# Kernel tuning notes

Measured on AMD Instinct MI355X. Metric: run time of the kernel, lower is better.

The kernel has to match this reference:

```python
import jax, jax.numpy as jnp
import numpy as np

B, S, D, H = 64, 197, 768, 12
HD = D // H  # 64
WIN = 14
NUM_REL = (2 * WIN - 1) ** 2 + 3  # 732


def _build_rel_index():
    ch = np.arange(WIN)
    coords = np.stack(np.meshgrid(ch, ch, indexing='ij'))  # [2, W, W]
    flat = coords.reshape(2, -1)  # [2, W*W]
    rel = flat[:, :, None] - flat[:, None, :]  # [2, W*W, W*W]
    rel = rel.transpose(1, 2, 0).astype(np.int64)
    rel[:, :, 0] += WIN - 1
    rel[:, :, 1] += WIN - 1
    rel[:, :, 0] *= 2 * WIN - 1
    idx = np.zeros((WIN * WIN + 1, WIN * WIN + 1), dtype=np.int64)
    idx[1:, 1:] = rel.sum(-1)
    idx[0, :] = NUM_REL - 3
    idx[:, 0] = NUM_REL - 2
    idx[0, 0] = NUM_REL - 1
    return idx


def setup_inputs() -> dict:
    key = jax.random.key(0)
    ks = jax.random.split(key, 7)
    s = 0.02
    return {
        'hidden_states': jax.random.normal(ks[0], (B, S, D), jnp.float32),
        'wq': jax.random.normal(ks[1], (D, D), jnp.float32) * s,
        'bq': jax.random.normal(ks[2], (D,), jnp.float32) * s,
        'wk': jax.random.normal(ks[3], (D, D), jnp.float32) * s,  # key has no bias in BEiT
        'wv': jax.random.normal(ks[4], (D, D), jnp.float32) * s,
        'bv': jax.random.normal(ks[5], (D,), jnp.float32) * s,
        'bias_table': jax.random.normal(ks[6], (NUM_REL, H), jnp.float32) * s,
        'rel_index': jnp.asarray(_build_rel_index(), jnp.int32),
    }


def reference(hidden_states, wq, bq, wk, wv, bv, bias_table, rel_index):
    def heads(x):  # [B,S,D] -> [B,H,S,HD]
        return x.reshape(B, S, H, HD).transpose(0, 2, 1, 3)

    q = heads(hidden_states @ wq.T + bq)
    k = heads(hidden_states @ wk.T)
    v = heads(hidden_states @ wv.T + bv)

    scale = 1.0 / jnp.sqrt(jnp.asarray(HD, hidden_states.dtype))
    scores = jnp.einsum('bhqd,bhkd->bhqk', q, k) * scale  # [B,H,S,S]

    # relative position bias: [S,S,H] -> [1,H,S,S]
    rel_bias = bias_table[rel_index].transpose(2, 0, 1)[None]
    scores = scores + rel_bias

    probs = jax.nn.softmax(scores, axis=-1)
    ctx = jnp.einsum('bhqk,bhkd->bhqd', probs, v)  # [B,H,S,HD]
    return ctx.transpose(0, 2, 1, 3).reshape(B, S, D)
```

## Files before the change

### kernel.cpp

```cpp
#include <hip/hip_runtime.h>


#define S_LEN 197
#define HEADS 12
#define HDIM 64
#define DMODEL 768
#define BATCH 64
#define MROWS (BATCH * S_LEN)
#define MPAD 12672
#define NCOLS (3 * DMODEL)
#define KDIM DMODEL
#define QKV_ELEMS ((size_t)BATCH * HEADS * S_LEN * HDIM)

#define NQT 13
#define SPAD 208
#define KS_STRIDE 72
#define VT_STRIDE 232
#define PS_STRIDE 232

typedef __attribute__((ext_vector_type(8))) short short8;
typedef __attribute__((ext_vector_type(4))) float floatx4;

__device__ __forceinline__ float bf2f(ushort u) {
  union { unsigned int i; float f; } x;
  x.i = ((unsigned int)u) << 16;
  return x.f;
}
__device__ __forceinline__ ushort f2bf(float f) {
  union { float f; unsigned int i; } x;
  x.f = f;
  unsigned int r = x.i + 0x7fffu + ((x.i >> 16) & 1u);
  return (ushort)(r >> 16);
}

__global__ void k_convert_h(const float* __restrict__ hs, ushort* __restrict__ hbf) {
  int col = blockIdx.x * 256 + threadIdx.x;
  int row = blockIdx.y;
  float v = (row < MROWS) ? hs[(size_t)row * DMODEL + col] : 0.f;
  hbf[(size_t)row * DMODEL + col] = f2bf(v);
}

__global__ void k_convert_w(const float* __restrict__ wq, const float* __restrict__ wk,
                            const float* __restrict__ wv, ushort* __restrict__ wbf) {
  int col = blockIdx.x * 256 + threadIdx.x;
  int row = blockIdx.y;
  const float* src = (row < DMODEL) ? &wq[(size_t)row * DMODEL]
                     : (row < 2 * DMODEL) ? &wk[(size_t)(row - DMODEL) * DMODEL]
                                          : &wv[(size_t)(row - 2 * DMODEL) * DMODEL];
  wbf[(size_t)row * DMODEL + col] = f2bf(src[col]);
}

__global__ void k_bias_expand(const float* __restrict__ bt, const int* __restrict__ ridx,
                              float* __restrict__ biasb) {
  int idx = blockIdx.x * 256 + threadIdx.x;
  if (idx >= HEADS * S_LEN * S_LEN) return;
  int h = idx / (S_LEN * S_LEN);
  int r = idx - h * (S_LEN * S_LEN);
  biasb[idx] = bt[ridx[r] * HEADS + h];
}

__global__ __launch_bounds__(256) void k_gemm_qkv(
    const ushort* __restrict__ A, const ushort* __restrict__ W,
    const float* __restrict__ bq, const float* __restrict__ bv,
    ushort* __restrict__ Qb, ushort* __restrict__ Kb, ushort* __restrict__ Vb) {
  __shared__ __align__(16) ushort As[128 * 40];
  __shared__ __align__(16) ushort Bs[128 * 40];
  int tid = threadIdx.x;
  int wave = tid >> 6, lane = tid & 63;
  int quad = lane >> 4, l16 = lane & 15;
  int m0 = blockIdx.y * 128, n0 = blockIdx.x * 128;
  int wm = (wave & 1) * 64, wn = (wave >> 1) * 64;

  floatx4 acc[4][4];
  floatx4 z = {0.f, 0.f, 0.f, 0.f};
#pragma unroll
  for (int i = 0; i < 4; ++i)
#pragma unroll
    for (int j = 0; j < 4; ++j) acc[i][j] = z;

  for (int kb = 0; kb < KDIM; kb += 32) {
#pragma unroll
    for (int s = 0; s < 2; ++s) {
      int c = tid + s * 256;
      int row = c >> 2;
      int kc = (c & 3) * 8;
      *(uint4*)(&As[row * 40 + kc]) =
          *(const uint4*)(&A[(size_t)(m0 + row) * KDIM + kb + kc]);
      *(uint4*)(&Bs[row * 40 + kc]) =
          *(const uint4*)(&W[(size_t)(n0 + row) * KDIM + kb + kc]);
    }
    __syncthreads();
    short8 af[4], bfr[4];
#pragma unroll
    for (int i = 0; i < 4; ++i) {
      af[i] = *(const short8*)(&As[(wm + i * 16 + l16) * 40 + quad * 8]);
      bfr[i] = *(const short8*)(&Bs[(wn + i * 16 + l16) * 40 + quad * 8]);
    }
#pragma unroll
    for (int i = 0; i < 4; ++i)
#pragma unroll
      for (int j = 0; j < 4; ++j)
        acc[i][j] = __builtin_amdgcn_mfma_f32_16x16x32_bf16(af[i], bfr[j], acc[i][j], 0, 0, 0);
    __syncthreads();
  }

#pragma unroll
  for (int j = 0; j < 4; ++j) {
    int col = n0 + wn + j * 16 + l16;
    int which = col / DMODEL;
    int rem = col - which * DMODEL;
    int hh = rem >> 6;
    int d = rem & 63;
    float bias = (which == 0) ? bq[col] : ((which == 2) ? bv[col - 2 * DMODEL] : 0.f);
    ushort* dst = (which == 0) ? Qb : ((which == 1) ? Kb : Vb);
#pragma unroll
    for (int i = 0; i < 4; ++i) {
#pragma unroll
      for (int r = 0; r < 4; ++r) {
        int m = m0 + wm + i * 16 + quad * 4 + r;
        if (m < MROWS) {
          int bb = m / S_LEN;
          int ss = m - bb * S_LEN;
          dst[((size_t)(bb * HEADS + hh) * S_LEN + ss) * HDIM + d] =
              f2bf(acc[i][j][r] + bias);
        }
      }
    }
  }
}

__global__ __launch_bounds__(512) void k_attn_mfma(
    const ushort* __restrict__ Qb, const ushort* __restrict__ Kb,
    const ushort* __restrict__ Vb, const float* __restrict__ biasb,
    float* __restrict__ out) {
  __shared__ __align__(16) ushort Ks[SPAD * KS_STRIDE];
  __shared__ __align__(16) ushort Vt[HDIM * VT_STRIDE];
  __shared__ __align__(16) ushort Ps[8 * 16 * PS_STRIDE];
  int bh = blockIdx.x;
  int b = bh / HEADS, h = bh - b * HEADS;
  int tid = threadIdx.x;
  int wave = tid >> 6, lane = tid & 63;
  int quad = lane >> 4, l16 = lane & 15;

  {
    uint4 z4 = {0u, 0u, 0u, 0u};
    for (int i = tid; i < SPAD * KS_STRIDE / 8; i += 512) ((uint4*)Ks)[i] = z4;
    for (int i = tid; i < HDIM * VT_STRIDE / 8; i += 512) ((uint4*)Vt)[i] = z4;
    for (int i = tid; i < 8 * 16 * PS_STRIDE / 8; i += 512) ((uint4*)Ps)[i] = z4;
  }
  __syncthreads();

  const ushort* Kg = Kb + (size_t)bh * S_LEN * HDIM;
  const ushort* Vg = Vb + (size_t)bh * S_LEN * HDIM;
  for (int idx = tid; idx < S_LEN * HDIM; idx += 512) {
    int key = idx >> 6, d = idx & 63;
    Ks[key * KS_STRIDE + d] = Kg[idx];
    Vt[d * VT_STRIDE + key] = Vg[idx];
  }
  __syncthreads();

  const ushort* Qg = Qb + (size_t)bh * S_LEN * HDIM;
  const float* biasH = biasb + (size_t)h * S_LEN * S_LEN;
  ushort* Psw = Ps + wave * 16 * PS_STRIDE;

  for (int qt = wave; qt < NQT; qt += 8) {
    int q0 = qt * 16;
    short8 qa0 = *(const short8*)&Qg[(q0 + l16) * HDIM + quad * 8];
    short8 qa1 = *(const short8*)&Qg[(q0 + l16) * HDIM + 32 + quad * 8];

    floatx4 brow[NQT];
    int qrow = q0 + quad * 4;
#pragma unroll
    for (int kt = 0; kt < NQT; ++kt) {
      int key = kt * 16 + l16;
      int keyc = (key < S_LEN) ? key : (S_LEN - 1);
#pragma unroll
      for (int r = 0; r < 4; ++r) {
        int q = qrow + r;
        int qc = (q < S_LEN) ? q : (S_LEN - 1);
        float bv = biasH[qc * S_LEN + keyc];
        brow[kt][r] = (q < S_LEN && key < S_LEN) ? bv : -1e30f;
      }
    }

    floatx4 sacc[NQT];
    floatx4 zz = {0.f, 0.f, 0.f, 0.f};
#pragma unroll
    for (int kt = 0; kt < NQT; ++kt) sacc[kt] = zz;
#pragma unroll
    for (int kt = 0; kt < NQT; ++kt) {
      short8 kb0 = *(const short8*)&Ks[(kt * 16 + l16) * KS_STRIDE + quad * 8];
      short8 kb1 = *(const short8*)&Ks[(kt * 16 + l16) * KS_STRIDE + 32 + quad * 8];
      sacc[kt] = __builtin_amdgcn_mfma_f32_16x16x32_bf16(qa0, kb0, sacc[kt], 0, 0, 0);
      sacc[kt] = __builtin_amdgcn_mfma_f32_16x16x32_bf16(qa1, kb1, sacc[kt], 0, 0, 0);
    }

    float mx[4] = {-3e38f, -3e38f, -3e38f, -3e38f};
#pragma unroll
    for (int kt = 0; kt < NQT; ++kt)
#pragma unroll
      for (int r = 0; r < 4; ++r) {
        float s = sacc[kt][r] * 0.125f + brow[kt][r];
        sacc[kt][r] = s;
        mx[r] = fmaxf(mx[r], s);
      }
#pragma unroll
    for (int r = 0; r < 4; ++r) {
      mx[r] = fmaxf(mx[r], __shfl_xor(mx[r], 1));
      mx[r] = fmaxf(mx[r], __shfl_xor(mx[r], 2));
      mx[r] = fmaxf(mx[r], __shfl_xor(mx[r], 4));
      mx[r] = fmaxf(mx[r], __shfl_xor(mx[r], 8));
    }
    float sum[4] = {0.f, 0.f, 0.f, 0.f};
#pragma unroll
    for (int kt = 0; kt < NQT; ++kt)
#pragma unroll
      for (int r = 0; r < 4; ++r) {
        float e = __expf(sacc[kt][r] - mx[r]);
        sum[r] += e;
        Psw[(quad * 4 + r) * PS_STRIDE + kt * 16 + l16] = f2bf(e);
      }
#pragma unroll
    for (int r = 0; r < 4; ++r) {
      sum[r] += __shfl_xor(sum[r], 1);
      sum[r] += __shfl_xor(sum[r], 2);
      sum[r] += __shfl_xor(sum[r], 4);
      sum[r] += __shfl_xor(sum[r], 8);
    }
    float inv[4];
#pragma unroll
    for (int r = 0; r < 4; ++r) inv[r] = 1.f / sum[r];

    floatx4 oacc[4];
#pragma unroll
    for (int dt = 0; dt < 4; ++dt) oacc[dt] = zz;
#pragma unroll
    for (int kk = 0; kk < 7; ++kk) {
      short8 pa = *(const short8*)&Psw[l16 * PS_STRIDE + kk * 32 + quad * 8];
#pragma unroll
      for (int dt = 0; dt < 4; ++dt) {
        short8 vb = *(const short8*)&Vt[(dt * 16 + l16) * VT_STRIDE + kk * 32 + quad * 8];
        oacc[dt] = __builtin_amdgcn_mfma_f32_16x16x32_bf16(pa, vb, oacc[dt], 0, 0, 0);
      }
    }

    float* outg = out + (size_t)b * S_LEN * DMODEL + h * HDIM;
#pragma unroll
    for (int dt = 0; dt < 4; ++dt) {
#pragma unroll
      for (int r = 0; r < 4; ++r) {
        int q = q0 + quad * 4 + r;
        if (q < S_LEN)
          outg[(size_t)q * DMODEL + dt * 16 + l16] = oacc[dt][r] * inv[r];
      }
    }
  }
}

extern "C" void kernel_launch(void* const* d_in, const int* in_sizes, int n_in,
                              void* d_out, int out_size, void* d_ws, size_t ws_size,
                              hipStream_t stream) {
  const float* hs = (const float*)d_in[0];
  const float* wq = (const float*)d_in[1];
  const float* bq = (const float*)d_in[2];
  const float* wk = (const float*)d_in[3];
  const float* wv = (const float*)d_in[4];
  const float* bv = (const float*)d_in[5];
  const float* bt = (const float*)d_in[6];
  const int* ridx = (const int*)d_in[7];
  float* out = (float*)d_out;

  ushort* hbf = (ushort*)d_ws;
  ushort* wbf = hbf + (size_t)MPAD * KDIM;
  ushort* Qb = wbf + (size_t)NCOLS * KDIM;
  ushort* Kb = Qb + QKV_ELEMS;
  ushort* Vb = Kb + QKV_ELEMS;
  float* biasb = (float*)(Vb + QKV_ELEMS);

  k_convert_h<<<dim3(3, MPAD), 256, 0, stream>>>(hs, hbf);
  k_convert_w<<<dim3(3, NCOLS), 256, 0, stream>>>(wq, wk, wv, wbf);
  int nb = (HEADS * S_LEN * S_LEN + 255) / 256;
  k_bias_expand<<<nb, 256, 0, stream>>>(bt, ridx, biasb);
  k_gemm_qkv<<<dim3(NCOLS / 128, MPAD / 128), 256, 0, stream>>>(hbf, wbf, bq, bv, Qb, Kb, Vb);
  k_attn_mfma<<<BATCH * HEADS, 512, 0, stream>>>(Qb, Kb, Vb, biasb, out);
}
```

Measured before the change: 251.4 us.

## Split attention key tiles across waves and use async LDS loads in QKV GEMM

The QKV GEMM now stages its tiles with global_load_lds direct-to-LDS loads into an XOR-swizzled 32-wide layout instead of padded register round-trips, and folds the 1/sqrt(d) scale into the Q projection. The attention kernel now has four waves cooperate on each 16-query tile, splitting the key tiles among them. K is read straight from global memory, the bias is fed in as the MFMA accumulator init, and the cross-wave max and sum reductions go through LDS with block barriers. V is transposed into a swizzled layout. The aim is more parallelism per query tile, fewer registers and less LDS traffic, at the cost of extra __syncthreads per iteration and uncached global K reads.

```diff
diff --git a/kernel.cpp b/kernel.cpp
--- a/kernel.cpp
+++ b/kernel.cpp
@@ -13,19 +13,17 @@
 #define QKV_ELEMS ((size_t)BATCH * HEADS * S_LEN * HDIM)
 
 #define NQT 13
-#define SPAD 208
-#define KS_STRIDE 72
-#define VT_STRIDE 232
-#define PS_STRIDE 232
+#define VT_ST 256
+#define P_ST 256
 
 typedef __attribute__((ext_vector_type(8))) short short8;
 typedef __attribute__((ext_vector_type(4))) float floatx4;
 
-__device__ __forceinline__ float bf2f(ushort u) {
-  union { unsigned int i; float f; } x;
-  x.i = ((unsigned int)u) << 16;
-  return x.f;
-}
+#define GLD16(gp, lp)                                                                  \
+  __builtin_amdgcn_global_load_lds(                                                    \
+      (const __attribute__((address_space(1))) unsigned int*)(gp),                     \
+      (__attribute__((address_space(3))) unsigned int*)(lp), 16, 0, 0)
+
 __device__ __forceinline__ ushort f2bf(float f) {
   union { float f; unsigned int i; } x;
   x.f = f;
@@ -63,13 +61,14 @@
     const ushort* __restrict__ A, const ushort* __restrict__ W,
     const float* __restrict__ bq, const float* __restrict__ bv,
     ushort* __restrict__ Qb, ushort* __restrict__ Kb, ushort* __restrict__ Vb) {
-  __shared__ __align__(16) ushort As[128 * 40];
-  __shared__ __align__(16) ushort Bs[128 * 40];
+  __shared__ __align__(16) ushort As[128 * 32];
+  __shared__ __align__(16) ushort Bs[128 * 32];
   int tid = threadIdx.x;
   int wave = tid >> 6, lane = tid & 63;
   int quad = lane >> 4, l16 = lane & 15;
   int m0 = blockIdx.y * 128, n0 = blockIdx.x * 128;
   int wm = (wave & 1) * 64, wn = (wave >> 1) * 64;
+  int swz = (quad ^ (l16 & 3)) << 3;
 
   floatx4 acc[4][4];
   floatx4 z = {0.f, 0.f, 0.f, 0.f};
@@ -78,23 +77,24 @@
 #pragma unroll
     for (int j = 0; j < 4; ++j) acc[i][j] = z;
 
+  int p0 = wave * 128 + lane;
   for (int kb = 0; kb < KDIM; kb += 32) {
+    const ushort* Arow = A + (size_t)m0 * KDIM + kb;
+    const ushort* Brow = W + (size_t)n0 * KDIM + kb;
 #pragma unroll
     for (int s = 0; s < 2; ++s) {
-      int c = tid + s * 256;
-      int row = c >> 2;
-      int kc = (c & 3) * 8;
-      *(uint4*)(&As[row * 40 + kc]) =
-          *(const uint4*)(&A[(size_t)(m0 + row) * KDIM + kb + kc]);
-      *(uint4*)(&Bs[row * 40 + kc]) =
-          *(const uint4*)(&W[(size_t)(n0 + row) * KDIM + kb + kc]);
+      int p = p0 + s * 64;
+      int r = p >> 2;
+      int kc = ((p ^ r) & 3) << 3;
+      GLD16(&Arow[(size_t)r * KDIM + kc], &As[p * 8]);
+      GLD16(&Brow[(size_t)r * KDIM + kc], &Bs[p * 8]);
     }
     __syncthreads();
     short8 af[4], bfr[4];
 #pragma unroll
     for (int i = 0; i < 4; ++i) {
-      af[i] = *(const short8*)(&As[(wm + i * 16 + l16) * 40 + quad * 8]);
-      bfr[i] = *(const short8*)(&Bs[(wn + i * 16 + l16) * 40 + quad * 8]);
+      af[i] = *(const short8*)(&As[(wm + i * 16 + l16) * 32 + swz]);
+      bfr[i] = *(const short8*)(&Bs[(wn + i * 16 + l16) * 32 + swz]);
     }
 #pragma unroll
     for (int i = 0; i < 4; ++i)
@@ -112,6 +112,7 @@
     int hh = rem >> 6;
     int d = rem & 63;
     float bias = (which == 0) ? bq[col] : ((which == 2) ? bv[col - 2 * DMODEL] : 0.f);
+    float scl = (which == 0) ? 0.125f : 1.0f;
     ushort* dst = (which == 0) ? Qb : ((which == 1) ? Kb : Vb);
 #pragma unroll
     for (int i = 0; i < 4; ++i) {
@@ -122,7 +123,7 @@
           int bb = m / S_LEN;
           int ss = m - bb * S_LEN;
           dst[((size_t)(bb * HEADS + hh) * S_LEN + ss) * HDIM + d] =
-              f2bf(acc[i][j][r] + bias);
+              f2bf((acc[i][j][r] + bias) * scl);
         }
       }
     }
@@ -133,125 +134,145 @@
     const ushort* __restrict__ Qb, const ushort* __restrict__ Kb,
     const ushort* __restrict__ Vb, const float* __restrict__ biasb,
     float* __restrict__ out) {
-  __shared__ __align__(16) ushort Ks[SPAD * KS_STRIDE];
-  __shared__ __align__(16) ushort Vt[HDIM * VT_STRIDE];
-  __shared__ __align__(16) ushort Ps[8 * 16 * PS_STRIDE];
+  __shared__ __align__(16) ushort Vt[HDIM * VT_ST];
+  __shared__ __align__(16) ushort Ps[2 * 16 * P_ST];
+  __shared__ __align__(16) float red[2 * 16 * 8];
   int bh = blockIdx.x;
   int b = bh / HEADS, h = bh - b * HEADS;
   int tid = threadIdx.x;
   int wave = tid >> 6, lane = tid & 63;
   int quad = lane >> 4, l16 = lane & 15;
+  int g = wave >> 2, wq = wave & 3;
 
   {
     uint4 z4 = {0u, 0u, 0u, 0u};
-    for (int i = tid; i < SPAD * KS_STRIDE / 8; i += 512) ((uint4*)Ks)[i] = z4;
-    for (int i = tid; i < HDIM * VT_STRIDE / 8; i += 512) ((uint4*)Vt)[i] = z4;
-    for (int i = tid; i < 8 * 16 * PS_STRIDE / 8; i += 512) ((uint4*)Ps)[i] = z4;
+    for (int i = tid; i < HDIM * VT_ST / 8; i += 512) ((uint4*)Vt)[i] = z4;
+    for (int i = tid; i < 2 * 16 * P_ST / 8; i += 512) ((uint4*)Ps)[i] = z4;
   }
   __syncthreads();
 
+  const ushort* Vg = Vb + (size_t)bh * S_LEN * HDIM;
+  for (int idx = tid; idx < S_LEN * 32; idx += 512) {
+    int key = idx >> 5;
+    int d = (idx & 31) * 2;
+    unsigned int v = *(const unsigned int*)&Vg[key * HDIM + d];
+    int co = key & 7, ch = key >> 3;
+    Vt[d * VT_ST + ((ch ^ (d & 7)) << 3) + co] = (ushort)(v & 0xffffu);
+    Vt[(d + 1) * VT_ST + ((ch ^ ((d + 1) & 7)) << 3) + co] = (ushort)(v >> 16);
+  }
+  __syncthreads();
+
+  const ushort* Qg = Qb + (size_t)bh * S_LEN * HDIM;
   const ushort* Kg = Kb + (size_t)bh * S_LEN * HDIM;
-  const ushort* Vg = Vb + (size_t)bh * S_LEN * HDIM;
-  for (int idx = tid; idx < S_LEN * HDIM; idx += 512) {
-    int key = idx >> 6, d = idx & 63;
-    Ks[key * KS_STRIDE + d] = Kg[idx];
-    Vt[d * VT_STRIDE + key] = Vg[idx];
-  }
-  __syncthreads();
-
-  const ushort* Qg = Qb + (size_t)bh * S_LEN * HDIM;
   const float* biasH = biasb + (size_t)h * S_LEN * S_LEN;
-  ushort* Psw = Ps + wave * 16 * PS_STRIDE;
-
-  for (int qt = wave; qt < NQT; qt += 8) {
-    int q0 = qt * 16;
-    short8 qa0 = *(const short8*)&Qg[(q0 + l16) * HDIM + quad * 8];
-    short8 qa1 = *(const short8*)&Qg[(q0 + l16) * HDIM + 32 + quad * 8];
-
-    floatx4 brow[NQT];
-    int qrow = q0 + quad * 4;
-#pragma unroll
-    for (int kt = 0; kt < NQT; ++kt) {
-      int key = kt * 16 + l16;
-      int keyc = (key < S_LEN) ? key : (S_LEN - 1);
-#pragma unroll
-      for (int r = 0; r < 4; ++r) {
-        int q = qrow + r;
-        int qc = (q < S_LEN) ? q : (S_LEN - 1);
-        float bv = biasH[qc * S_LEN + keyc];
-        brow[kt][r] = (q < S_LEN && key < S_LEN) ? bv : -1e30f;
-      }
-    }
-
-    floatx4 sacc[NQT];
-    floatx4 zz = {0.f, 0.f, 0.f, 0.f};
-#pragma unroll
-    for (int kt = 0; kt < NQT; ++kt) sacc[kt] = zz;
-#pragma unroll
-    for (int kt = 0; kt < NQT; ++kt) {
-      short8 kb0 = *(const short8*)&Ks[(kt * 16 + l16) * KS_STRIDE + quad * 8];
-      short8 kb1 = *(const short8*)&Ks[(kt * 16 + l16) * KS_STRIDE + 32 + quad * 8];
-      sacc[kt] = __builtin_amdgcn_mfma_f32_16x16x32_bf16(qa0, kb0, sacc[kt], 0, 0, 0);
-      sacc[kt] = __builtin_amdgcn_mfma_f32_16x16x32_bf16(qa1, kb1, sacc[kt], 0, 0, 0);
-    }
-
-    float mx[4] = {-3e38f, -3e38f, -3e38f, -3e38f};
-#pragma unroll
-    for (int kt = 0; kt < NQT; ++kt)
-#pragma unroll
-      for (int r = 0; r < 4; ++r) {
-        float s = sacc[kt][r] * 0.125f + brow[kt][r];
-        sacc[kt][r] = s;
-        mx[r] = fmaxf(mx[r], s);
-      }
-#pragma unroll
-    for (int r = 0; r < 4; ++r) {
-      mx[r] = fmaxf(mx[r], __shfl_xor(mx[r], 1));
-      mx[r] = fmaxf(mx[r], __shfl_xor(mx[r], 2));
-      mx[r] = fmaxf(mx[r], __shfl_xor(mx[r], 4));
-      mx[r] = fmaxf(mx[r], __shfl_xor(mx[r], 8));
-    }
-    float sum[4] = {0.f, 0.f, 0.f, 0.f};
-#pragma unroll
-    for (int kt = 0; kt < NQT; ++kt)
-#pragma unroll
-      for (int r = 0; r < 4; ++r) {
-        float e = __expf(sacc[kt][r] - mx[r]);
-        sum[r] += e;
-        Psw[(quad * 4 + r) * PS_STRIDE + kt * 16 + l16] = f2bf(e);
-      }
-#pragma unroll
-    for (int r = 0; r < 4; ++r) {
-      sum[r] += __shfl_xor(sum[r], 1);
-      sum[r] += __shfl_xor(sum[r], 2);
-      sum[r] += __shfl_xor(sum[r], 4);
-      sum[r] += __shfl_xor(sum[r], 8);
-    }
-    float inv[4];
-#pragma unroll
-    for (int r = 0; r < 4; ++r) inv[r] = 1.f / sum[r];
-
-    floatx4 oacc[4];
-#pragma unroll
-    for (int dt = 0; dt < 4; ++dt) oacc[dt] = zz;
-#pragma unroll
-    for (int kk = 0; kk < 7; ++kk) {
-      short8 pa = *(const short8*)&Psw[l16 * PS_STRIDE + kk * 32 + quad * 8];
-#pragma unroll
-      for (int dt = 0; dt < 4; ++dt) {
-        short8 vb = *(const short8*)&Vt[(dt * 16 + l16) * VT_STRIDE + kk * 32 + quad * 8];
-        oacc[dt] = __builtin_amdgcn_mfma_f32_16x16x32_bf16(pa, vb, oacc[dt], 0, 0, 0);
-      }
-    }
-
-    float* outg = out + (size_t)b * S_LEN * DMODEL + h * HDIM;
-#pragma unroll
-    for (int dt = 0; dt < 4; ++dt) {
-#pragma unroll
-      for (int r = 0; r < 4; ++r) {
-        int q = q0 + quad * 4 + r;
-        if (q < S_LEN)
-          outg[(size_t)q * DMODEL + dt * 16 + l16] = oacc[dt][r] * inv[r];
+  ushort* Pg = Ps + g * 16 * P_ST;
+  float* redg = red + g * 16 * 8;
+  int kt0 = (wq == 0) ? 0 : (3 * wq + 1);
+  int ktn = (wq == 0) ? 4 : 3;
+
+  for (int it = 0; it < 7; ++it) {
+    int qt = 2 * it + g;
+    bool active = (qt < NQT);
+    floatx4 sacc[4];
+    float mx[4];
+    if (active) {
+      int q0 = qt * 16;
+      short8 qa0 = *(const short8*)&Qg[(q0 + l16) * HDIM + quad * 8];
+      short8 qa1 = *(const short8*)&Qg[(q0 + l16) * HDIM + 32 + quad * 8];
+      int qrow = q0 + quad * 4;
+#pragma unroll
+      for (int t = 0; t < 4; ++t) {
+        if (t < ktn) {
+          int key = (kt0 + t) * 16 + l16;
+          int keyc = (key < S_LEN) ? key : (S_LEN - 1);
+          floatx4 cin;
+#pragma unroll
+          for (int r = 0; r < 4; ++r) {
+            int q = qrow + r;
+            int qc = (q < S_LEN) ? q : (S_LEN - 1);
+            float bv = biasH[qc * S_LEN + keyc];
+            cin[r] = (q < S_LEN && key < S_LEN) ? bv : -1e30f;
+          }
+          short8 kb0 = *(const short8*)&Kg[key * HDIM + quad * 8];
+          short8 kb1 = *(const short8*)&Kg[key * HDIM + 32 + quad * 8];
+          floatx4 s1 = __builtin_amdgcn_mfma_f32_16x16x32_bf16(qa0, kb0, cin, 0, 0, 0);
+          sacc[t] = __builtin_amdgcn_mfma_f32_16x16x32_bf16(qa1, kb1, s1, 0, 0, 0);
+        }
+      }
+#pragma unroll
+      for (int r = 0; r < 4; ++r) {
+        float m = -3e38f;
+#pragma unroll
+        for (int t = 0; t < 4; ++t)
+          if (t < ktn) m = fmaxf(m, sacc[t][r]);
+        m = fmaxf(m, __shfl_xor(m, 1));
+        m = fmaxf(m, __shfl_xor(m, 2));
+        m = fmaxf(m, __shfl_xor(m, 4));
+        m = fmaxf(m, __shfl_xor(m, 8));
+        mx[r] = m;
+      }
+      if (l16 == 0) {
+#pragma unroll
+        for (int r = 0; r < 4; ++r) redg[(quad * 4 + r) * 8 + wq] = mx[r];
+      }
+    }
+    __syncthreads();
+    if (active) {
+      float sum[4];
+#pragma unroll
+      for (int r = 0; r < 4; ++r) {
+        floatx4 mp = *(const floatx4*)&redg[(quad * 4 + r) * 8];
+        mx[r] = fmaxf(fmaxf(mp[0], mp[1]), fmaxf(mp[2], mp[3]));
+        sum[r] = 0.f;
+      }
+#pragma unroll
+      for (int t = 0; t < 4; ++t) {
+        if (t < ktn) {
+          int col = (kt0 + t) * 16 + l16;
+          int cpos = col >> 3, coff = col & 7;
+#pragma unroll
+          for (int r = 0; r < 4; ++r) {
+            int row = quad * 4 + r;
+            float e = __expf(sacc[t][r] - mx[r]);
+            sum[r] += e;
+            Pg[row * P_ST + ((cpos ^ (row & 7)) << 3) + coff] = f2bf(e);
+          }
+        }
+      }
+#pragma unroll
+      for (int r = 0; r < 4; ++r) {
+        float s = sum[r];
+        s += __shfl_xor(s, 1);
+        s += __shfl_xor(s, 2);
+        s += __shfl_xor(s, 4);
+        s += __shfl_xor(s, 8);
+        sum[r] = s;
+      }
+      if (l16 == 0) {
+#pragma unroll
+        for (int r = 0; r < 4; ++r) redg[(quad * 4 + r) * 8 + 4 + wq] = sum[r];
+      }
+    }
+    __syncthreads();
+    if (active) {
+      floatx4 oacc = {0.f, 0.f, 0.f, 0.f};
+      int d = wq * 16 + l16;
+#pragma unroll
+      for (int kk = 0; kk < 7; ++kk) {
+        int cidx = 4 * kk + quad;
+        short8 pa = *(const short8*)&Pg[l16 * P_ST + ((cidx ^ (l16 & 7)) << 3)];
+        short8 vb2 = *(const short8*)&Vt[d * VT_ST + ((cidx ^ (d & 7)) << 3)];
+        oacc = __builtin_amdgcn_mfma_f32_16x16x32_bf16(pa, vb2, oacc, 0, 0, 0);
+      }
+      int q0 = qt * 16;
+      float* outg = out + (size_t)b * S_LEN * DMODEL + h * HDIM + d;
+#pragma unroll
+      for (int r = 0; r < 4; ++r) {
+        int row = quad * 4 + r;
+        floatx4 sp = *(const floatx4*)&redg[row * 8 + 4];
+        float tot = sp[0] + sp[1] + sp[2] + sp[3];
+        int q = q0 + row;
+        if (q < S_LEN) outg[(size_t)q * DMODEL] = oacc[r] * (1.f / tot);
       }
     }
   }
```

Result: slower. 283.9 us (+12.9%).
